# Kernel tuning notes

Hardware: AMD Instinct MI355X
Metric: run time of the kernel (lower is better)

## Reference

```python
import jax, jax.numpy as jnp
import numpy as np


def setup_inputs() -> dict:
    key = jax.random.key(0)
    ks = jax.random.split(key, 8)
    B, N, D = 8, 2048, 128
    s = 1.0 / float(np.sqrt(D))
    node = jax.random.normal(ks[0], (B, N, D), dtype=jnp.float32)
    node_mask = jax.random.randint(ks[1], (B, N), 0, 2, dtype=jnp.int32)
    punctuation_graph = jax.random.randint(ks[2], (B, N, N), 0, 2, dtype=jnp.int32)
    w_nw = jax.random.uniform(ks[3], (1, D), jnp.float32, -s, s)
    b_nw = jax.random.uniform(ks[4], (1,), jnp.float32, -s, s)
    w_self = jax.random.uniform(ks[5], (D, D), jnp.float32, -s, s)
    b_self = jax.random.uniform(ks[6], (D,), jnp.float32, -s, s)
    w_punct = jax.random.uniform(ks[7], (D, D), jnp.float32, -s, s)
    return {"node": node, "node_mask": node_mask, "punctuation_graph": punctuation_graph,
            "w_nw": w_nw, "b_nw": b_nw, "w_self": w_self, "b_self": b_self,
            "w_punct": w_punct, "iteration_steps": 2}


def reference(node, node_mask, punctuation_graph, w_nw, b_nw, w_self, b_self, w_punct, iteration_steps):
    B, N, D = node.shape
    # dd_graph = mask outer product with zeroed diagonal; graph = dd_graph * punctuation_graph
    eye = jnp.eye(N, dtype=punctuation_graph.dtype)
    dd = node_mask[:, None, :] * node_mask[:, :, None] * (1 - eye)[None, :, :]  # [B,N,N]
    graph = dd * punctuation_graph  # [B,N,N] int, binary
    nbr_num = graph.sum(-1)  # [B,N]
    # replace_masked_values(nbr_num, nbr_num>=1, 1): nodes with no neighbors get denom 1
    nbr_f = jnp.where(nbr_num >= 1, nbr_num.astype(node.dtype), jnp.asarray(1.0, node.dtype))
    gmask = graph > 0
    weights = []
    x = node
    for _ in range(iteration_steps):  # small fixed step count
        dw = jax.nn.sigmoid(jnp.einsum('bnd,od->bno', x, w_nw) + b_nw)[..., 0]  # [B,N]
        weights.append(dw)
        self_info = jnp.einsum('bnd,ed->bne', x, w_self) + b_self  # [B,N,D]
        info_p = jnp.einsum('bnd,ed->bne', x, w_punct)  # [B,N,D]
        # node_weight[b,i,j] = dw[b,j] where graph[b,i,j] else 0
        nw = jnp.where(gmask, dw[:, None, :], jnp.asarray(0.0, x.dtype))  # [B,N,N]
        agg = jnp.einsum('bnm,bmd->bnd', nw, info_p) / nbr_f[..., None]
        x = jax.nn.relu(self_info + agg)
    all_weight = jnp.stack(weights, axis=1)  # [B, steps, N]
    return x, all_weight
```

## Files before the change

kernel.cpp:

```cpp
#include <hip/hip_runtime.h>
#include <hip/hip_bf16.h>

#define BB 8
#define NN 2048
#define DD 128

typedef __attribute__((ext_vector_type(8))) __bf16 bf16x8;
typedef __attribute__((ext_vector_type(4))) float f32x4;
typedef __attribute__((ext_vector_type(4))) int   i32x4;

static __device__ __forceinline__ unsigned short f2bf(float f) {
    union { float f; unsigned u; } v; v.f = f;
    unsigned r = (v.u + 0x7FFFu + ((v.u >> 16) & 1u)) >> 16;
    return (unsigned short)r;
}
static __device__ __forceinline__ float bf2f(unsigned short b) {
    union { unsigned u; float f; } v; v.u = ((unsigned)b) << 16;
    return v.f;
}

__global__ __launch_bounds__(256) void kernP(
    const int* __restrict__ punct, const int* __restrict__ mask,
    const float* __restrict__ w_self, const float* __restrict__ w_punct,
    unsigned* __restrict__ pk, float* __restrict__ scale_g, float* __restrict__ pdm_g,
    unsigned short* __restrict__ wc)
{
    const int t = threadIdx.x;
    if (blockIdx.x == 4096) {
        for (int idx = t; idx < 128 * 256; idx += 256) {
            const int e = idx >> 8, k = idx & 255;
            const float v = (k < 128) ? w_self[e * 128 + k]
                                      : w_punct[e * 128 + (k - 128)];
            wc[idx] = f2bf(v);
        }
        return;
    }
    const int wave = t >> 6, lane = t & 63;
    const int row_g = blockIdx.x * 4 + wave;
    const int b = row_g >> 11;
    const int i = row_g & (NN - 1);

    const int* prow = punct + (size_t)row_g * NN;
    const int* mrow = mask + (size_t)b * NN;

    unsigned pk0 = 0, pk1 = 0;
    int acc = 0;
    #pragma unroll 4
    for (int w = 0; w < 32; ++w) {
        const int col = w * 64 + lane;
        const int pred = (prow[col] & mrow[col]) & 1;
        unsigned long long bal = __ballot(pred);
        if (lane == w) { pk0 = (unsigned)bal; pk1 = (unsigned)(bal >> 32); }
        acc += pred + ((col == i ? pred : 0) << 16);
    }
    #pragma unroll
    for (int o = 32; o > 0; o >>= 1) acc += __shfl_xor(acc, o, 64);

    if (lane < 32) {
        uint2 w2; w2.x = pk0; w2.y = pk1;
        *(uint2*)(pk + (size_t)row_g * 64 + 2 * lane) = w2;
    }
    if (lane == 0) {
        const int nall = acc & 0xFFFF;
        const int pdm  = acc >> 16;
        const int mi   = mrow[i];
        const int nbr  = nall - pdm;
        scale_g[row_g] = mi ? 1.f / (float)(nbr < 1 ? 1 : nbr) : 0.f;
        pdm_g[row_g]   = (float)pdm;
    }
}

__global__ __launch_bounds__(256) void kernD(
    const float* __restrict__ x,
    const float* __restrict__ w_nw, const float* __restrict__ b_nw,
    float* __restrict__ aw_out,
    unsigned short* __restrict__ xbf, unsigned short* __restrict__ xw,
    unsigned short* __restrict__ xwT)
{
    __shared__ float wnw_l[DD];
    __shared__ float red[256];
    __shared__ float dw_l[64];
    __shared__ unsigned short xl[64 * 136];

    const int t  = threadIdx.x;
    const int n0 = blockIdx.x * 64;
    const int b  = n0 >> 11;
    const int nb = n0 & (NN - 1);

    if (t < DD) wnw_l[t] = w_nw[t];
    __syncthreads();

    const int row = t >> 2, q = t & 3;
    const float* xs = x + (size_t)(n0 + row) * DD + q * 32;
    float vals[32];
    float dp = 0.f;
    #pragma unroll
    for (int j = 0; j < 8; ++j) {
        f32x4 a = *(const f32x4*)(xs + j * 4);
        vals[j*4+0] = a.x; vals[j*4+1] = a.y; vals[j*4+2] = a.z; vals[j*4+3] = a.w;
        const float* wv = &wnw_l[q * 32 + j * 4];
        dp += a.x*wv[0] + a.y*wv[1] + a.z*wv[2] + a.w*wv[3];
    }
    red[t] = dp;
    __syncthreads();
    if (t < 64) {
        float s = red[4*t] + red[4*t+1] + red[4*t+2] + red[4*t+3] + b_nw[0];
        float dv = 1.f / (1.f + __expf(-s));
        dw_l[t] = dv;
        aw_out[(size_t)b * 2 * NN + nb + t] = dv;
    }
    __syncthreads();

    unsigned pb[16];
    #pragma unroll
    for (int j = 0; j < 16; ++j)
        pb[j] = f2bf(vals[2*j]) | ((unsigned)f2bf(vals[2*j+1]) << 16);
    {
        i32x4* dst = (i32x4*)(xbf + (size_t)(n0 + row) * DD + q * 32);
        i32x4 v0 = {(int)pb[0],(int)pb[1],(int)pb[2],(int)pb[3]};
        i32x4 v1 = {(int)pb[4],(int)pb[5],(int)pb[6],(int)pb[7]};
        i32x4 v2 = {(int)pb[8],(int)pb[9],(int)pb[10],(int)pb[11]};
        i32x4 v3 = {(int)pb[12],(int)pb[13],(int)pb[14],(int)pb[15]};
        dst[0]=v0; dst[1]=v1; dst[2]=v2; dst[3]=v3;
    }
    const float dwv = dw_l[row];
    #pragma unroll
    for (int j = 0; j < 16; ++j)
        pb[j] = f2bf(vals[2*j]*dwv) | ((unsigned)f2bf(vals[2*j+1]*dwv) << 16);
    {
        i32x4 v0 = {(int)pb[0],(int)pb[1],(int)pb[2],(int)pb[3]};
        i32x4 v1 = {(int)pb[4],(int)pb[5],(int)pb[6],(int)pb[7]};
        i32x4 v2 = {(int)pb[8],(int)pb[9],(int)pb[10],(int)pb[11]};
        i32x4 v3 = {(int)pb[12],(int)pb[13],(int)pb[14],(int)pb[15]};
        i32x4* dst = (i32x4*)(xw + (size_t)(n0 + row) * DD + q * 32);
        dst[0]=v0; dst[1]=v1; dst[2]=v2; dst[3]=v3;
        i32x4* ld = (i32x4*)&xl[row * 136 + q * 32];
        ld[0]=v0; ld[1]=v1; ld[2]=v2; ld[3]=v3;
    }
    __syncthreads();
    {
        const int d = t >> 1, half = t & 1;
        unsigned o[16];
        #pragma unroll
        for (int k = 0; k < 16; ++k) {
            const int r0 = half * 32 + 2 * k;
            o[k] = (unsigned)xl[r0 * 136 + d] | ((unsigned)xl[(r0+1) * 136 + d] << 16);
        }
        i32x4 v0 = {(int)o[0],(int)o[1],(int)o[2],(int)o[3]};
        i32x4 v1 = {(int)o[4],(int)o[5],(int)o[6],(int)o[7]};
        i32x4 v2 = {(int)o[8],(int)o[9],(int)o[10],(int)o[11]};
        i32x4 v3 = {(int)o[12],(int)o[13],(int)o[14],(int)o[15]};
        i32x4* dst = (i32x4*)(xwT + (size_t)(b * DD + d) * NN + nb + half * 32);
        dst[0]=v0; dst[1]=v1; dst[2]=v2; dst[3]=v3;
    }
}

__global__ __launch_bounds__(256) void kernE(
    const unsigned* __restrict__ pk,
    const float* __restrict__ scale_g, const float* __restrict__ pdm_g,
    const unsigned short* __restrict__ xwT,
    const unsigned short* __restrict__ xw,
    const unsigned short* __restrict__ xbf,
    const unsigned short* __restrict__ wc,
    const float* __restrict__ b_self,
    const float* __restrict__ w_nw, const float* __restrict__ b_nw,
    float* __restrict__ x_out, float* __restrict__ aw_next,
    unsigned short* __restrict__ xbf_o, unsigned short* __restrict__ xw_o,
    unsigned short* __restrict__ xwT_o)
{
    __shared__ unsigned pPk[64 * 68];
    __shared__ unsigned short ZsL[64 * 136];
    __shared__ float scale_l[64], pdm_l[64], dw_l[64];

    const int t  = threadIdx.x;
    const int b  = blockIdx.x >> 5;
    const int i0 = (blockIdx.x & 31) * 64;
    const size_t rg0 = (size_t)b * NN + i0;

    #pragma unroll
    for (int r = 0; r < 4; ++r) {
        const int u = r * 256 + t;
        const int row = u >> 4;
        const int wq  = (u & 15) * 4;
        i32x4 v = *(const i32x4*)(pk + (rg0 + row) * 64 + wq);
        *(i32x4*)&pPk[row * 68 + wq] = v;
    }
    if (t < 64) {
        scale_l[t] = scale_g[rg0 + t];
        pdm_l[t]   = pdm_g[rg0 + t];
    }
    __syncthreads();

    const int wn = t >> 6, lane = t & 63;
    const int quad = lane >> 4, l16 = lane & 15;
    const unsigned short* xwTb = xwT + (size_t)b * DD * NN;

    f32x4 acc[4][2] = {};
    #pragma unroll 4
    for (int kk = 0; kk < 64; ++kk) {
        bf16x8 bfr[2];
        #pragma unroll
        for (int nt = 0; nt < 2; ++nt) {
            const int d = wn*32 + nt*16 + l16;
            bfr[nt] = *(const bf16x8*)(xwTb + (size_t)d * NN + kk*32 + quad*8);
        }
        bf16x8 af[4];
        #pragma unroll
        for (int mt = 0; mt < 4; ++mt) {
            const unsigned w = pPk[(mt*16 + l16) * 68 + kk];
            const unsigned by = (w >> (quad * 8)) & 0xFFu;
            i32x4 ex;
            ex.x = ((by &   1u) ? 0x3F80 : 0) | ((by &   2u) ? 0x3F800000 : 0);
            ex.y = ((by &   4u) ? 0x3F80 : 0) | ((by &   8u) ? 0x3F800000 : 0);
            ex.z = ((by &  16u) ? 0x3F80 : 0) | ((by &  32u) ? 0x3F800000 : 0);
            ex.w = ((by &  64u) ? 0x3F80 : 0) | ((by & 128u) ? 0x3F800000 : 0);
            union { i32x4 i; bf16x8 h; } cv; cv.i = ex;
            af[mt] = cv.h;
        }
        #pragma unroll
        for (int mt = 0; mt < 4; ++mt)
            #pragma unroll
            for (int nt = 0; nt < 2; ++nt)
                acc[mt][nt] = __builtin_amdgcn_mfma_f32_16x16x32_bf16(af[mt], bfr[nt], acc[mt][nt], 0, 0, 0);
    }

    #pragma unroll
    for (int mt = 0; mt < 4; ++mt) {
        #pragma unroll
        for (int nt = 0; nt < 2; ++nt) {
            const int d = wn*32 + nt*16 + l16;
            #pragma unroll
            for (int r = 0; r < 4; ++r) {
                const int row = mt*16 + quad*4 + r;
                const float xwv = bf2f(xw[(rg0 + row) * DD + d]);
                const float zs = scale_l[row] * (acc[mt][nt][r] - pdm_l[row] * xwv);
                ZsL[row * 136 + d] = f2bf(zs);
            }
        }
    }
    __syncthreads();

    f32x4 acc2[4][2] = {};
    #pragma unroll
    for (int kq2 = 0; kq2 < 8; ++kq2) {
        bf16x8 b2[2];
        #pragma unroll
        for (int nt2 = 0; nt2 < 2; ++nt2) {
            const int e = wn*32 + nt2*16 + l16;
            b2[nt2] = *(const bf16x8*)(wc + (size_t)e * 256 + kq2*32 + quad*8);
        }
        bf16x8 a2[4];
        if (kq2 < 4) {
            #pragma unroll
            for (int mt = 0; mt < 4; ++mt)
                a2[mt] = *(const bf16x8*)(xbf + (rg0 + mt*16 + l16) * DD + kq2*32 + quad*8);
        } else {
            #pragma unroll
            for (int mt = 0; mt < 4; ++mt)
                a2[mt] = *(const bf16x8*)&ZsL[(mt*16 + l16) * 136 + (kq2-4)*32 + quad*8];
        }
        #pragma unroll
        for (int mt = 0; mt < 4; ++mt)
            #pragma unroll
            for (int nt2 = 0; nt2 < 2; ++nt2)
                acc2[mt][nt2] = __builtin_amdgcn_mfma_f32_16x16x32_bf16(a2[mt], b2[nt2], acc2[mt][nt2], 0, 0, 0);
    }
    __syncthreads();

    float bias[2], wnv[2];
    #pragma unroll
    for (int nt2 = 0; nt2 < 2; ++nt2) {
        const int e = wn*32 + nt2*16 + l16;
        bias[nt2] = b_self[e];
        wnv[nt2]  = w_nw[e];
    }
    float* red = (float*)pPk;
    #pragma unroll
    for (int mt = 0; mt < 4; ++mt) {
        #pragma unroll
        for (int r = 0; r < 4; ++r) {
            const int row = mt*16 + quad*4 + r;
            float p = 0.f;
            #pragma unroll
            for (int nt2 = 0; nt2 < 2; ++nt2) {
                const int e = wn*32 + nt2*16 + l16;
                float v = fmaxf(acc2[mt][nt2][r] + bias[nt2], 0.f);
                acc2[mt][nt2][r] = v;
                x_out[(rg0 + row) * DD + e] = v;
                ZsL[row * 136 + e] = f2bf(v);
                p += v * wnv[nt2];
            }
            red[row * 65 + wn*16 + l16] = p;
        }
    }
    __syncthreads();
    if (t < 64) {
        float s = b_nw[0];
        #pragma unroll 8
        for (int c = 0; c < 64; ++c) s += red[t * 65 + c];
        float dv = 1.f / (1.f + __expf(-s));
        dw_l[t] = dv;
        aw_next[(size_t)b * 2 * NN + i0 + t] = dv;
    }
    __syncthreads();

    {
        const int row = t >> 2, q = t & 3;
        const i32x4* src = (const i32x4*)&ZsL[row * 136 + q * 32];
        i32x4 u0 = src[0], u1 = src[1], u2 = src[2], u3 = src[3];
        i32x4* db = (i32x4*)(xbf_o + (rg0 + row) * DD + q * 32);
        db[0]=u0; db[1]=u1; db[2]=u2; db[3]=u3;
        const float dwv = dw_l[row];
        unsigned uu[8] = {(unsigned)u0.x,(unsigned)u0.y,(unsigned)u0.z,(unsigned)u0.w,
                          (unsigned)u1.x,(unsigned)u1.y,(unsigned)u1.z,(unsigned)u1.w};
        unsigned vv[8] = {(unsigned)u2.x,(unsigned)u2.y,(unsigned)u2.z,(unsigned)u2.w,
                          (unsigned)u3.x,(unsigned)u3.y,(unsigned)u3.z,(unsigned)u3.w};
        unsigned o[16];
        #pragma unroll
        for (int j = 0; j < 8; ++j) {
            float lo = bf2f((unsigned short)(uu[j] & 0xFFFF)) * dwv;
            float hi = bf2f((unsigned short)(uu[j] >> 16)) * dwv;
            o[j] = f2bf(lo) | ((unsigned)f2bf(hi) << 16);
        }
        #pragma unroll
        for (int j = 0; j < 8; ++j) {
            float lo = bf2f((unsigned short)(vv[j] & 0xFFFF)) * dwv;
            float hi = bf2f((unsigned short)(vv[j] >> 16)) * dwv;
            o[8+j] = f2bf(lo) | ((unsigned)f2bf(hi) << 16);
        }
        i32x4 w0 = {(int)o[0],(int)o[1],(int)o[2],(int)o[3]};
        i32x4 w1 = {(int)o[4],(int)o[5],(int)o[6],(int)o[7]};
        i32x4 w2 = {(int)o[8],(int)o[9],(int)o[10],(int)o[11]};
        i32x4 w3 = {(int)o[12],(int)o[13],(int)o[14],(int)o[15]};
        i32x4* dw_ = (i32x4*)(xw_o + (rg0 + row) * DD + q * 32);
        dw_[0]=w0; dw_[1]=w1; dw_[2]=w2; dw_[3]=w3;
        i32x4* lw = (i32x4*)&ZsL[row * 136 + q * 32];
        __syncthreads();
        lw[0]=w0; lw[1]=w1; lw[2]=w2; lw[3]=w3;
    }
    __syncthreads();
    {
        const int d = t >> 1, half = t & 1;
        unsigned o[16];
        #pragma unroll
        for (int k = 0; k < 16; ++k) {
            const int r0 = half * 32 + 2 * k;
            o[k] = (unsigned)ZsL[r0 * 136 + d] | ((unsigned)ZsL[(r0+1) * 136 + d] << 16);
        }
        i32x4 v0 = {(int)o[0],(int)o[1],(int)o[2],(int)o[3]};
        i32x4 v1 = {(int)o[4],(int)o[5],(int)o[6],(int)o[7]};
        i32x4 v2 = {(int)o[8],(int)o[9],(int)o[10],(int)o[11]};
        i32x4 v3 = {(int)o[12],(int)o[13],(int)o[14],(int)o[15]};
        i32x4* dst = (i32x4*)(xwT_o + (size_t)(b * DD + d) * NN + i0 + half * 32);
        dst[0]=v0; dst[1]=v1; dst[2]=v2; dst[3]=v3;
    }
}

extern "C" void kernel_launch(void* const* d_in, const int* in_sizes, int n_in,
                              void* d_out, int out_size, void* d_ws, size_t ws_size,
                              hipStream_t stream) {
    const float* node   = (const float*)d_in[0];
    const int*   mask   = (const int*)  d_in[1];
    const int*   punct  = (const int*)  d_in[2];
    const float* w_nw   = (const float*)d_in[3];
    const float* b_nw   = (const float*)d_in[4];
    const float* w_self = (const float*)d_in[5];
    const float* b_self = (const float*)d_in[6];
    const float* w_punct= (const float*)d_in[7];

    float* xout = (float*)d_out;
    float* aw   = xout + (size_t)BB * NN * DD;

    char* w = (char*)d_ws;
    unsigned*       pk    = (unsigned*)w;
    float*          scl   = (float*)(w + (4u<<20));
    float*          pdm   = (float*)(w + (4u<<20) + (64u<<10));
    unsigned short* wc    = (unsigned short*)(w + (4u<<20) + (128u<<10));
    float*          awdum = (float*)(w + (4u<<20) + (192u<<10));
    unsigned short* xbf0  = (unsigned short*)(w + (5u<<20));
    unsigned short* xw0   = (unsigned short*)(w + (9u<<20));
    unsigned short* xwT0  = (unsigned short*)(w + (13u<<20));
    unsigned short* xbf1  = (unsigned short*)(w + (17u<<20));
    unsigned short* xw1   = (unsigned short*)(w + (21u<<20));
    unsigned short* xwT1  = (unsigned short*)(w + (25u<<20));

    dim3 blk(256);
    kernP<<<dim3(4097), blk, 0, stream>>>(punct, mask, w_self, w_punct, pk, scl, pdm, wc);
    kernD<<<dim3(256), blk, 0, stream>>>(node, w_nw, b_nw, aw, xbf0, xw0, xwT0);
    kernE<<<dim3(256), blk, 0, stream>>>(pk, scl, pdm, xwT0, xw0, xbf0, wc, b_self,
                                         w_nw, b_nw, xout, aw + NN, xbf1, xw1, xwT1);
    kernE<<<dim3(256), blk, 0, stream>>>(pk, scl, pdm, xwT1, xw1, xbf1, wc, b_self,
                                         w_nw, b_nw, xout, awdum, xbf0, xw0, xwT0);
}
```

Measured before the change: 317.8 us.

## Split aggregation and projection kernels, vectorize graph bit-packing, drop diagonal correction

```diff
diff --git a/kernel.cpp b/kernel.cpp
--- a/kernel.cpp
+++ b/kernel.cpp
@@ -22,7 +22,7 @@
 __global__ __launch_bounds__(256) void kernP(
     const int* __restrict__ punct, const int* __restrict__ mask,
     const float* __restrict__ w_self, const float* __restrict__ w_punct,
-    unsigned* __restrict__ pk, float* __restrict__ scale_g, float* __restrict__ pdm_g,
+    unsigned* __restrict__ pk, float* __restrict__ scale_g,
     unsigned short* __restrict__ wc)
 {
     const int t = threadIdx.x;
@@ -40,33 +40,27 @@
     const int b = row_g >> 11;
     const int i = row_g & (NN - 1);
 
-    const int* prow = punct + (size_t)row_g * NN;
-    const int* mrow = mask + (size_t)b * NN;
-
-    unsigned pk0 = 0, pk1 = 0;
-    int acc = 0;
-    #pragma unroll 4
-    for (int w = 0; w < 32; ++w) {
-        const int col = w * 64 + lane;
-        const int pred = (prow[col] & mrow[col]) & 1;
-        unsigned long long bal = __ballot(pred);
-        if (lane == w) { pk0 = (unsigned)bal; pk1 = (unsigned)(bal >> 32); }
-        acc += pred + ((col == i ? pred : 0) << 16);
-    }
-    #pragma unroll
-    for (int o = 32; o > 0; o >>= 1) acc += __shfl_xor(acc, o, 64);
-
-    if (lane < 32) {
-        uint2 w2; w2.x = pk0; w2.y = pk1;
-        *(uint2*)(pk + (size_t)row_g * 64 + 2 * lane) = w2;
-    }
+    const int* prow = punct + (size_t)row_g * NN + lane * 32;
+    const int* mrow = mask + (size_t)b * NN + lane * 32;
+
+    unsigned pp = 0, mm = 0;
+    #pragma unroll
+    for (int c = 0; c < 8; ++c) {
+        i32x4 pv = *(const i32x4*)(prow + c * 4);
+        i32x4 mv = *(const i32x4*)(mrow + c * 4);
+        pp |= (unsigned)((pv.x & 1) | ((pv.y & 1) << 1) | ((pv.z & 1) << 2) | ((pv.w & 1) << 3)) << (c * 4);
+        mm |= (unsigned)((mv.x & 1) | ((mv.y & 1) << 1) | ((mv.z & 1) << 2) | ((mv.w & 1) << 3)) << (c * 4);
+    }
+    unsigned pw = pp & mm;
+    if (lane == (i >> 5)) pw &= ~(1u << (i & 31));
+    pk[(size_t)row_g * 64 + lane] = pw;
+
+    int cnt = __popc(pw);
+    #pragma unroll
+    for (int o = 32; o > 0; o >>= 1) cnt += __shfl_xor(cnt, o, 64);
     if (lane == 0) {
-        const int nall = acc & 0xFFFF;
-        const int pdm  = acc >> 16;
-        const int mi   = mrow[i];
-        const int nbr  = nall - pdm;
-        scale_g[row_g] = mi ? 1.f / (float)(nbr < 1 ? 1 : nbr) : 0.f;
-        pdm_g[row_g]   = (float)pdm;
+        const int mi = mask[(size_t)b * NN + i];
+        scale_g[row_g] = mi ? 1.f / (float)(cnt < 1 ? 1 : cnt) : 0.f;
     }
 }
 
@@ -74,8 +68,7 @@
     const float* __restrict__ x,
     const float* __restrict__ w_nw, const float* __restrict__ b_nw,
     float* __restrict__ aw_out,
-    unsigned short* __restrict__ xbf, unsigned short* __restrict__ xw,
-    unsigned short* __restrict__ xwT)
+    unsigned short* __restrict__ ab, unsigned short* __restrict__ xwT)
 {
     __shared__ float wnw_l[DD];
     __shared__ float red[256];
@@ -116,7 +109,7 @@
     for (int j = 0; j < 16; ++j)
         pb[j] = f2bf(vals[2*j]) | ((unsigned)f2bf(vals[2*j+1]) << 16);
     {
-        i32x4* dst = (i32x4*)(xbf + (size_t)(n0 + row) * DD + q * 32);
+        i32x4* dst = (i32x4*)(ab + (size_t)(n0 + row) * 256 + q * 32);
         i32x4 v0 = {(int)pb[0],(int)pb[1],(int)pb[2],(int)pb[3]};
         i32x4 v1 = {(int)pb[4],(int)pb[5],(int)pb[6],(int)pb[7]};
         i32x4 v2 = {(int)pb[8],(int)pb[9],(int)pb[10],(int)pb[11]};
@@ -132,8 +125,6 @@
         i32x4 v1 = {(int)pb[4],(int)pb[5],(int)pb[6],(int)pb[7]};
         i32x4 v2 = {(int)pb[8],(int)pb[9],(int)pb[10],(int)pb[11]};
         i32x4 v3 = {(int)pb[12],(int)pb[13],(int)pb[14],(int)pb[15]};
-        i32x4* dst = (i32x4*)(xw + (size_t)(n0 + row) * DD + q * 32);
-        dst[0]=v0; dst[1]=v1; dst[2]=v2; dst[3]=v3;
         i32x4* ld = (i32x4*)&xl[row * 136 + q * 32];
         ld[0]=v0; ld[1]=v1; ld[2]=v2; ld[3]=v3;
     }
@@ -155,47 +146,35 @@
     }
 }
 
-__global__ __launch_bounds__(256) void kernE(
-    const unsigned* __restrict__ pk,
-    const float* __restrict__ scale_g, const float* __restrict__ pdm_g,
+__global__ __launch_bounds__(256) void kernC2(
+    const unsigned* __restrict__ pk, const float* __restrict__ scale_g,
     const unsigned short* __restrict__ xwT,
-    const unsigned short* __restrict__ xw,
-    const unsigned short* __restrict__ xbf,
-    const unsigned short* __restrict__ wc,
-    const float* __restrict__ b_self,
-    const float* __restrict__ w_nw, const float* __restrict__ b_nw,
-    float* __restrict__ x_out, float* __restrict__ aw_next,
-    unsigned short* __restrict__ xbf_o, unsigned short* __restrict__ xw_o,
-    unsigned short* __restrict__ xwT_o)
+    unsigned short* __restrict__ ab)
 {
-    __shared__ unsigned pPk[64 * 68];
-    __shared__ unsigned short ZsL[64 * 136];
-    __shared__ float scale_l[64], pdm_l[64], dw_l[64];
+    __shared__ unsigned pPk[32 * 68];
+    __shared__ float scale_l[32];
 
     const int t  = threadIdx.x;
-    const int b  = blockIdx.x >> 5;
-    const int i0 = (blockIdx.x & 31) * 64;
+    const int b  = blockIdx.x >> 6;
+    const int i0 = (blockIdx.x & 63) * 32;
     const size_t rg0 = (size_t)b * NN + i0;
 
     #pragma unroll
-    for (int r = 0; r < 4; ++r) {
+    for (int r = 0; r < 2; ++r) {
         const int u = r * 256 + t;
         const int row = u >> 4;
         const int wq  = (u & 15) * 4;
         i32x4 v = *(const i32x4*)(pk + (rg0 + row) * 64 + wq);
         *(i32x4*)&pPk[row * 68 + wq] = v;
     }
-    if (t < 64) {
-        scale_l[t] = scale_g[rg0 + t];
-        pdm_l[t]   = pdm_g[rg0 + t];
-    }
+    if (t < 32) scale_l[t] = scale_g[rg0 + t];
     __syncthreads();
 
     const int wn = t >> 6, lane = t & 63;
     const int quad = lane >> 4, l16 = lane & 15;
     const unsigned short* xwTb = xwT + (size_t)b * DD * NN;
 
-    f32x4 acc[4][2] = {};
+    f32x4 acc[2][2] = {};
     #pragma unroll 4
     for (int kk = 0; kk < 64; ++kk) {
         bf16x8 bfr[2];
@@ -204,9 +183,9 @@
             const int d = wn*32 + nt*16 + l16;
             bfr[nt] = *(const bf16x8*)(xwTb + (size_t)d * NN + kk*32 + quad*8);
         }
-        bf16x8 af[4];
-        #pragma unroll
-        for (int mt = 0; mt < 4; ++mt) {
+        bf16x8 af[2];
+        #pragma unroll
+        for (int mt = 0; mt < 2; ++mt) {
             const unsigned w = pPk[(mt*16 + l16) * 68 + kk];
             const unsigned by = (w >> (quad * 8)) & 0xFFu;
             i32x4 ex;
@@ -218,63 +197,75 @@
             af[mt] = cv.h;
         }
         #pragma unroll
-        for (int mt = 0; mt < 4; ++mt)
+        for (int mt = 0; mt < 2; ++mt)
             #pragma unroll
             for (int nt = 0; nt < 2; ++nt)
                 acc[mt][nt] = __builtin_amdgcn_mfma_f32_16x16x32_bf16(af[mt], bfr[nt], acc[mt][nt], 0, 0, 0);
     }
 
     #pragma unroll
-    for (int mt = 0; mt < 4; ++mt) {
+    for (int mt = 0; mt < 2; ++mt) {
         #pragma unroll
         for (int nt = 0; nt < 2; ++nt) {
             const int d = wn*32 + nt*16 + l16;
             #pragma unroll
             for (int r = 0; r < 4; ++r) {
                 const int row = mt*16 + quad*4 + r;
-                const float xwv = bf2f(xw[(rg0 + row) * DD + d]);
-                const float zs = scale_l[row] * (acc[mt][nt][r] - pdm_l[row] * xwv);
-                ZsL[row * 136 + d] = f2bf(zs);
+                ab[(rg0 + row) * 256 + 128 + d] = f2bf(scale_l[row] * acc[mt][nt][r]);
             }
         }
     }
-    __syncthreads();
-
-    f32x4 acc2[4][2] = {};
-    #pragma unroll
-    for (int kq2 = 0; kq2 < 8; ++kq2) {
+}
+
+__global__ __launch_bounds__(256) void kernF(
+    const unsigned short* __restrict__ ab,
+    const unsigned short* __restrict__ wc,
+    const float* __restrict__ b_self,
+    const float* __restrict__ w_nw, const float* __restrict__ b_nw,
+    float* __restrict__ x_out, float* __restrict__ aw_next,
+    unsigned short* __restrict__ ab_next, unsigned short* __restrict__ xwT_next,
+    int want_next)
+{
+    __shared__ unsigned short xl[64 * 136];
+    __shared__ float red[64 * 65];
+    __shared__ float dw_l[64];
+
+    const int t  = threadIdx.x;
+    const int n0 = blockIdx.x * 64;
+    const int b  = n0 >> 11;
+    const int nb = n0 & (NN - 1);
+    const size_t rg0 = (size_t)n0;
+
+    const int wn = t >> 6, lane = t & 63;
+    const int quad = lane >> 4, l16 = lane & 15;
+
+    f32x4 acc[4][2] = {};
+    #pragma unroll
+    for (int kq = 0; kq < 8; ++kq) {
         bf16x8 b2[2];
         #pragma unroll
-        for (int nt2 = 0; nt2 < 2; ++nt2) {
-            const int e = wn*32 + nt2*16 + l16;
-            b2[nt2] = *(const bf16x8*)(wc + (size_t)e * 256 + kq2*32 + quad*8);
+        for (int nt = 0; nt < 2; ++nt) {
+            const int e = wn*32 + nt*16 + l16;
+            b2[nt] = *(const bf16x8*)(wc + (size_t)e * 256 + kq*32 + quad*8);
         }
         bf16x8 a2[4];
-        if (kq2 < 4) {
-            #pragma unroll
-            for (int mt = 0; mt < 4; ++mt)
-                a2[mt] = *(const bf16x8*)(xbf + (rg0 + mt*16 + l16) * DD + kq2*32 + quad*8);
-        } else {
-            #pragma unroll
-            for (int mt = 0; mt < 4; ++mt)
-                a2[mt] = *(const bf16x8*)&ZsL[(mt*16 + l16) * 136 + (kq2-4)*32 + quad*8];
-        }
         #pragma unroll
         for (int mt = 0; mt < 4; ++mt)
-            #pragma unroll
-            for (int nt2 = 0; nt2 < 2; ++nt2)
-                acc2[mt][nt2] = __builtin_amdgcn_mfma_f32_16x16x32_bf16(a2[mt], b2[nt2], acc2[mt][nt2], 0, 0, 0);
-    }
-    __syncthreads();
+            a2[mt] = *(const bf16x8*)(ab + (rg0 + mt*16 + l16) * 256 + kq*32 + quad*8);
+        #pragma unroll
+        for (int mt = 0; mt < 4; ++mt)
+            #pragma unroll
+            for (int nt = 0; nt < 2; ++nt)
+                acc[mt][nt] = __builtin_amdgcn_mfma_f32_16x16x32_bf16(a2[mt], b2[nt], acc[mt][nt], 0, 0, 0);
+    }
 
     float bias[2], wnv[2];
     #pragma unroll
-    for (int nt2 = 0; nt2 < 2; ++nt2) {
-        const int e = wn*32 + nt2*16 + l16;
-        bias[nt2] = b_self[e];
-        wnv[nt2]  = w_nw[e];
-    }
-    float* red = (float*)pPk;
+    for (int nt = 0; nt < 2; ++nt) {
+        const int e = wn*32 + nt*16 + l16;
+        bias[nt] = b_self[e];
+        wnv[nt]  = w_nw[e];
+    }
     #pragma unroll
     for (int mt = 0; mt < 4; ++mt) {
         #pragma unroll
@@ -282,13 +273,12 @@
             const int row = mt*16 + quad*4 + r;
             float p = 0.f;
             #pragma unroll
-            for (int nt2 = 0; nt2 < 2; ++nt2) {
-                const int e = wn*32 + nt2*16 + l16;
-                float v = fmaxf(acc2[mt][nt2][r] + bias[nt2], 0.f);
-                acc2[mt][nt2][r] = v;
+            for (int nt = 0; nt < 2; ++nt) {
+                const int e = wn*32 + nt*16 + l16;
+                float v = fmaxf(acc[mt][nt][r] + bias[nt], 0.f);
                 x_out[(rg0 + row) * DD + e] = v;
-                ZsL[row * 136 + e] = f2bf(v);
-                p += v * wnv[nt2];
+                xl[row * 136 + e] = f2bf(v);
+                p += v * wnv[nt];
             }
             red[row * 65 + wn*16 + l16] = p;
         }
@@ -300,59 +290,35 @@
         for (int c = 0; c < 64; ++c) s += red[t * 65 + c];
         float dv = 1.f / (1.f + __expf(-s));
         dw_l[t] = dv;
-        aw_next[(size_t)b * 2 * NN + i0 + t] = dv;
-    }
-    __syncthreads();
-
-    {
-        const int row = t >> 2, q = t & 3;
-        const i32x4* src = (const i32x4*)&ZsL[row * 136 + q * 32];
-        i32x4 u0 = src[0], u1 = src[1], u2 = src[2], u3 = src[3];
-        i32x4* db = (i32x4*)(xbf_o + (rg0 + row) * DD + q * 32);
-        db[0]=u0; db[1]=u1; db[2]=u2; db[3]=u3;
-        const float dwv = dw_l[row];
-        unsigned uu[8] = {(unsigned)u0.x,(unsigned)u0.y,(unsigned)u0.z,(unsigned)u0.w,
-                          (unsigned)u1.x,(unsigned)u1.y,(unsigned)u1.z,(unsigned)u1.w};
-        unsigned vv[8] = {(unsigned)u2.x,(unsigned)u2.y,(unsigned)u2.z,(unsigned)u2.w,
-                          (unsigned)u3.x,(unsigned)u3.y,(unsigned)u3.z,(unsigned)u3.w};
-        unsigned o[16];
-        #pragma unroll
-        for (int j = 0; j < 8; ++j) {
-            float lo = bf2f((unsigned short)(uu[j] & 0xFFFF)) * dwv;
-            float hi = bf2f((unsigned short)(uu[j] >> 16)) * dwv;
-            o[j] = f2bf(lo) | ((unsigned)f2bf(hi) << 16);
-        }
-        #pragma unroll
-        for (int j = 0; j < 8; ++j) {
-            float lo = bf2f((unsigned short)(vv[j] & 0xFFFF)) * dwv;
-            float hi = bf2f((unsigned short)(vv[j] >> 16)) * dwv;
-            o[8+j] = f2bf(lo) | ((unsigned)f2bf(hi) << 16);
-        }
-        i32x4 w0 = {(int)o[0],(int)o[1],(int)o[2],(int)o[3]};
-        i32x4 w1 = {(int)o[4],(int)o[5],(int)o[6],(int)o[7]};
-        i32x4 w2 = {(int)o[8],(int)o[9],(int)o[10],(int)o[11]};
-        i32x4 w3 = {(int)o[12],(int)o[13],(int)o[14],(int)o[15]};
-        i32x4* dw_ = (i32x4*)(xw_o + (rg0 + row) * DD + q * 32);
-        dw_[0]=w0; dw_[1]=w1; dw_[2]=w2; dw_[3]=w3;
-        i32x4* lw = (i32x4*)&ZsL[row * 136 + q * 32];
-        __syncthreads();
-        lw[0]=w0; lw[1]=w1; lw[2]=w2; lw[3]=w3;
-    }
-    __syncthreads();
-    {
-        const int d = t >> 1, half = t & 1;
-        unsigned o[16];
-        #pragma unroll
-        for (int k = 0; k < 16; ++k) {
-            const int r0 = half * 32 + 2 * k;
-            o[k] = (unsigned)ZsL[r0 * 136 + d] | ((unsigned)ZsL[(r0+1) * 136 + d] << 16);
-        }
-        i32x4 v0 = {(int)o[0],(int)o[1],(int)o[2],(int)o[3]};
-        i32x4 v1 = {(int)o[4],(int)o[5],(int)o[6],(int)o[7]};
-        i32x4 v2 = {(int)o[8],(int)o[9],(int)o[10],(int)o[11]};
-        i32x4 v3 = {(int)o[12],(int)o[13],(int)o[14],(int)o[15]};
-        i32x4* dst = (i32x4*)(xwT_o + (size_t)(b * DD + d) * NN + i0 + half * 32);
-        dst[0]=v0; dst[1]=v1; dst[2]=v2; dst[3]=v3;
+        aw_next[(size_t)b * 2 * NN + nb + t] = dv;
+    }
+    __syncthreads();
+
+    if (want_next) {
+        {
+            const int row = t >> 2, q = t & 3;
+            const i32x4* src = (const i32x4*)&xl[row * 136 + q * 32];
+            i32x4 v0 = src[0], v1 = src[1], v2 = src[2], v3 = src[3];
+            i32x4* dst = (i32x4*)(ab_next + (rg0 + row) * 256 + q * 32);
+            dst[0]=v0; dst[1]=v1; dst[2]=v2; dst[3]=v3;
+        }
+        {
+            const int d = t >> 1, half = t & 1;
+            unsigned o[16];
+            #pragma unroll
+            for (int k = 0; k < 16; ++k) {
+                const int r0 = half * 32 + 2 * k;
+                const float lo = bf2f(xl[r0 * 136 + d]) * dw_l[r0];
+                const float hi = bf2f(xl[(r0+1) * 136 + d]) * dw_l[r0+1];
+                o[k] = f2bf(lo) | ((unsigned)f2bf(hi) << 16);
+            }
+            i32x4 v0 = {(int)o[0],(int)o[1],(int)o[2],(int)o[3]};
+            i32x4 v1 = {(int)o[4],(int)o[5],(int)o[6],(int)o[7]};
+            i32x4 v2 = {(int)o[8],(int)o[9],(int)o[10],(int)o[11]};
+            i32x4 v3 = {(int)o[12],(int)o[13],(int)o[14],(int)o[15]};
+            i32x4* dst = (i32x4*)(xwT_next + (size_t)(b * DD + d) * NN + nb + half * 32);
+            dst[0]=v0; dst[1]=v1; dst[2]=v2; dst[3]=v3;
+        }
     }
 }
 
@@ -374,21 +340,20 @@
     char* w = (char*)d_ws;
     unsigned*       pk    = (unsigned*)w;
     float*          scl   = (float*)(w + (4u<<20));
-    float*          pdm   = (float*)(w + (4u<<20) + (64u<<10));
-    unsigned short* wc    = (unsigned short*)(w + (4u<<20) + (128u<<10));
-    float*          awdum = (float*)(w + (4u<<20) + (192u<<10));
-    unsigned short* xbf0  = (unsigned short*)(w + (5u<<20));
-    unsigned short* xw0   = (unsigned short*)(w + (9u<<20));
-    unsigned short* xwT0  = (unsigned short*)(w + (13u<<20));
-    unsigned short* xbf1  = (unsigned short*)(w + (17u<<20));
-    unsigned short* xw1   = (unsigned short*)(w + (21u<<20));
+    unsigned short* wc    = (unsigned short*)(w + (4u<<20) + (64u<<10));
+    float*          awdum = (float*)(w + (4u<<20) + (128u<<10));
+    unsigned short* ab0   = (unsigned short*)(w + (5u<<20));
+    unsigned short* ab1   = (unsigned short*)(w + (13u<<20));
+    unsigned short* xwT0  = (unsigned short*)(w + (21u<<20));
     unsigned short* xwT1  = (unsigned short*)(w + (25u<<20));
 
     dim3 blk(256);
-    kernP<<<dim3(4097), blk, 0, stream>>>(punct, mask, w_self, w_punct, pk, scl, pdm, wc);
-    kernD<<<dim3(256), blk, 0, stream>>>(node, w_nw, b_nw, aw, xbf0, xw0, xwT0);
-    kernE<<<dim3(256), blk, 0, stream>>>(pk, scl, pdm, xwT0, xw0, xbf0, wc, b_self,
-                                         w_nw, b_nw, xout, aw + NN, xbf1, xw1, xwT1);
-    kernE<<<dim3(256), blk, 0, stream>>>(pk, scl, pdm, xwT1, xw1, xbf1, wc, b_self,
-                                         w_nw, b_nw, xout, awdum, xbf0, xw0, xwT0);
-}
+    kernP<<<dim3(4097), blk, 0, stream>>>(punct, mask, w_self, w_punct, pk, scl, wc);
+    kernD<<<dim3(256), blk, 0, stream>>>(node, w_nw, b_nw, aw, ab0, xwT0);
+    kernC2<<<dim3(512), blk, 0, stream>>>(pk, scl, xwT0, ab0);
+    kernF<<<dim3(256), blk, 0, stream>>>(ab0, wc, b_self, w_nw, b_nw,
+                                         xout, aw + NN, ab1, xwT1, 1);
+    kernC2<<<dim3(512), blk, 0, stream>>>(pk, scl, xwT1, ab1);
+    kernF<<<dim3(256), blk, 0, stream>>>(ab1, wc, b_self, w_nw, b_nw,
+                                         xout, awdum, ab0, xwT0, 0);
+}
```

Result: slower. 335.5 us (+5.6%).
